# Performance work log

Hardware: AMD Instinct MI355X
Metric: run time of the kernel (lower is better)

## Reference

```python
import jax, jax.numpy as jnp
import numpy as np

N_I = 500_000   # 'indivi' nodes (dst)
N_H = 200_000   # 'house' nodes
F_I = 32        # indivi feature dim
F_H = 16        # house feature dim
EF = 8          # edge_attr dim
E1 = 2_000_000  # house->indivi edges
E2 = 2_000_000  # indivi->indivi edges


def setup_inputs() -> dict:
    key = jax.random.key(0)
    ks = jax.random.split(key, 16)
    return {
        "x_indivi": jax.random.normal(ks[0], (N_I, F_I), jnp.float32),
        "x_house": jax.random.normal(ks[1], (N_H, F_H), jnp.float32),
        "edge_attr_h2i": jax.random.normal(ks[2], (E1, EF), jnp.float32),
        "edge_attr_i2i": jax.random.normal(ks[3], (E2, EF), jnp.float32),
        "W_edge_h2i": jax.random.normal(ks[4], (F_H, EF), jnp.float32) * 0.1,
        "b_edge_h2i": jax.random.normal(ks[5], (F_H,), jnp.float32) * 0.1,
        "W_edge_i2i": jax.random.normal(ks[6], (F_I, EF), jnp.float32) * 0.1,
        "b_edge_i2i": jax.random.normal(ks[7], (F_I,), jnp.float32) * 0.1,
        "W_root_h2i": jax.random.normal(ks[8], (1, F_I), jnp.float32) * 0.1,
        "bias_h2i": jax.random.normal(ks[9], (1,), jnp.float32) * 0.1,
        "W_root_i2i": jax.random.normal(ks[10], (1, F_I), jnp.float32) * 0.1,
        "bias_i2i": jax.random.normal(ks[11], (1,), jnp.float32) * 0.1,
        "src_h2i": jax.random.randint(ks[12], (E1,), 0, N_H, jnp.int32),
        "dst_h2i": jax.random.randint(ks[13], (E1,), 0, N_I, jnp.int32),
        "src_i2i": jax.random.randint(ks[14], (E2,), 0, N_I, jnp.int32),
        "dst_i2i": jax.random.randint(ks[15], (E2,), 0, N_I, jnp.int32),
    }


def _nnconv(x_src, x_dst, edge_attr, src, dst, W_edge, b_edge, W_root, bias, num_dst):
    # Edge MLP -> per-edge weight matrix of shape [F_src, out=1], flattened to [E, F_src]
    w = edge_attr @ W_edge.T + b_edge                     # [E, F_src]
    # message_e = x_src[src_e] @ w_e  (out_channels = 1)
    msg = jnp.sum(x_src[src] * w, axis=-1, keepdims=True)  # [E, 1]
    agg = jax.ops.segment_sum(msg, dst, num_segments=num_dst)  # [N_dst, 1]
    # root transform on destination features + bias
    return agg + x_dst @ W_root.T + bias                  # [N_dst, 1]


def reference(x_indivi, x_house, edge_attr_h2i, edge_attr_i2i,
              W_edge_h2i, b_edge_h2i, W_edge_i2i, b_edge_i2i,
              W_root_h2i, bias_h2i, W_root_i2i, bias_i2i,
              src_h2i, dst_h2i, src_i2i, dst_i2i):
    out_h = _nnconv(x_house, x_indivi, edge_attr_h2i, src_h2i, dst_h2i,
                    W_edge_h2i, b_edge_h2i, W_root_h2i, bias_h2i, N_I)
    out_i = _nnconv(x_indivi, x_indivi, edge_attr_i2i, src_i2i, dst_i2i,
                    W_edge_i2i, b_edge_i2i, W_root_i2i, bias_i2i, N_I)
    # HeteroConv(aggr='sum') over the two relations targeting 'indivi'
    return out_h + out_i
```

## Files before the change

### kernel.cpp

```cpp
#include <hip/hip_runtime.h>

#define N_I 500000
#define N_H 200000
#define E1  2000000
#define E2  2000000
#define TOTAL_E (E1 + E2)

#define NB 512
#define CHUNK 2048
#define NWG ((TOTAL_E + CHUNK - 1) / CHUNK)
#define NB_RED ((N_I + 1023) / 1024)
#define WPT 8

template<int F, bool ROOT>
__global__ __launch_bounds__(256) void precompute_g(
    const float* __restrict__ x, const float* __restrict__ W, const float* __restrict__ b,
    float* __restrict__ g, int n,
    const float* __restrict__ rW1, const float* __restrict__ rW2,
    const float* __restrict__ rb1, const float* __restrict__ rb2,
    float* __restrict__ out)
{
    __shared__ float Wf[F * 8];
    __shared__ float bv[F];
    __shared__ float wr[F];

    for (int i = threadIdx.x; i < F * 8; i += 256) Wf[i] = W[i];
    if (threadIdx.x < F) {
        bv[threadIdx.x] = b[threadIdx.x];
        if (ROOT) wr[threadIdx.x] = rW1[threadIdx.x] + rW2[threadIdx.x];
    }
    __syncthreads();

    int nid = blockIdx.x * 256 + threadIdx.x;
    if (nid >= n) return;

    float xv[F];
    const float4* xp = (const float4*)(x + (size_t)nid * F);
    #pragma unroll
    for (int q = 0; q < F / 4; q++) {
        float4 v = xp[q];
        xv[q*4+0] = v.x; xv[q*4+1] = v.y; xv[q*4+2] = v.z; xv[q*4+3] = v.w;
    }

    float acc[9];
    #pragma unroll
    for (int k = 0; k < 9; k++) acc[k] = 0.f;

    #pragma unroll
    for (int j = 0; j < F; j++) {
        float4 w0 = *(const float4*)(Wf + j * 8);
        float4 w1 = *(const float4*)(Wf + j * 8 + 4);
        float xj = xv[j];
        acc[0] = fmaf(xj, w0.x, acc[0]);
        acc[1] = fmaf(xj, w0.y, acc[1]);
        acc[2] = fmaf(xj, w0.z, acc[2]);
        acc[3] = fmaf(xj, w0.w, acc[3]);
        acc[4] = fmaf(xj, w1.x, acc[4]);
        acc[5] = fmaf(xj, w1.y, acc[5]);
        acc[6] = fmaf(xj, w1.z, acc[6]);
        acc[7] = fmaf(xj, w1.w, acc[7]);
        acc[8] = fmaf(xj, bv[j], acc[8]);
    }

    float4* gp = (float4*)(g + (size_t)nid * 12);
    gp[0] = make_float4(acc[0], acc[1], acc[2], acc[3]);
    gp[1] = make_float4(acc[4], acc[5], acc[6], acc[7]);
    gp[2] = make_float4(acc[8], 0.f, 0.f, 0.f);

    if (ROOT) {
        float r = rb1[0] + rb2[0];
        #pragma unroll
        for (int j = 0; j < F; j++) r = fmaf(xv[j], wr[j], r);
        out[nid] = r;
    }
}

__device__ __forceinline__ void edge_msg(
    int t,
    const int* __restrict__ src1, const int* __restrict__ dst1,
    const float* __restrict__ ea1, const float* __restrict__ g1,
    const int* __restrict__ src2, const int* __restrict__ dst2,
    const float* __restrict__ ea2, const float* __restrict__ g2,
    int& d_out, float& m_out)
{
    const int* srcp; const int* dstp; const float* eap; const float* gp;
    int e;
    if (t < E1) { e = t;      srcp = src1; dstp = dst1; eap = ea1; gp = g1; }
    else        { e = t - E1; srcp = src2; dstp = dst2; eap = ea2; gp = g2; }

    int s = srcp[e];
    d_out = dstp[e];
    const float4* ap = (const float4*)(eap + (size_t)e * 8);
    float4 a0 = ap[0];
    float4 a1 = ap[1];
    const float4* gr = (const float4*)(gp + (size_t)s * 12);
    float4 ga = gr[0];
    float4 gb = gr[1];
    float4 gc = gr[2];

    float msg = gc.x;
    msg = fmaf(a0.x, ga.x, msg);
    msg = fmaf(a0.y, ga.y, msg);
    msg = fmaf(a0.z, ga.z, msg);
    msg = fmaf(a0.w, ga.w, msg);
    msg = fmaf(a1.x, gb.x, msg);
    msg = fmaf(a1.y, gb.y, msg);
    msg = fmaf(a1.z, gb.z, msg);
    msg = fmaf(a1.w, gb.w, msg);
    m_out = msg;
}

__global__ __launch_bounds__(256) void hist_kernel(
    const int* __restrict__ dst1, const int* __restrict__ dst2,
    int* __restrict__ H)
{
    __shared__ int hist[NB];
    for (int i = threadIdx.x; i < NB; i += 256) hist[i] = 0;
    __syncthreads();

    int base = blockIdx.x * CHUNK;
    #pragma unroll
    for (int it = 0; it < CHUNK / 256; ++it) {
        int t = base + it * 256 + threadIdx.x;
        if (t < TOTAL_E) {
            int d = (t < E1) ? dst1[t] : dst2[t - E1];
            atomicAdd(&hist[d >> 10], 1);
        }
    }
    __syncthreads();
    for (int i = threadIdx.x; i < NB; i += 256) H[blockIdx.x * NB + i] = hist[i];
}

__global__ __launch_bounds__(256) void scan_cols_kernel(int* __restrict__ H,
                                                        int* __restrict__ total)
{
    __shared__ int sums[256];
    int b = blockIdx.x;
    int tid = threadIdx.x;

    int vals[WPT];
    int s = 0;
    #pragma unroll
    for (int k = 0; k < WPT; k++) {
        int w = tid * WPT + k;
        vals[k] = (w < NWG) ? H[w * NB + b] : 0;
        s += vals[k];
    }
    sums[tid] = s;
    __syncthreads();
    for (int off = 1; off < 256; off <<= 1) {
        int t = (tid >= off) ? sums[tid - off] : 0;
        __syncthreads();
        sums[tid] += t;
        __syncthreads();
    }
    int run = sums[tid] - s;
    #pragma unroll
    for (int k = 0; k < WPT; k++) {
        int w = tid * WPT + k;
        if (w < NWG) H[w * NB + b] = run;
        run += vals[k];
    }
    if (tid == 255) total[b] = sums[255];
}

__global__ __launch_bounds__(512) void scan_base_kernel(const int* __restrict__ total,
                                                        int* __restrict__ base)
{
    __shared__ int v[512];
    int tid = threadIdx.x;
    int orig = total[tid];
    v[tid] = orig;
    __syncthreads();
    for (int off = 1; off < 512; off <<= 1) {
        int t = (tid >= off) ? v[tid - off] : 0;
        __syncthreads();
        v[tid] += t;
        __syncthreads();
    }
    base[tid] = v[tid] - orig;
}

__global__ __launch_bounds__(256) void scatter_msg_kernel(
    const int* __restrict__ src1, const int* __restrict__ dst1,
    const float* __restrict__ ea1, const float* __restrict__ g1,
    const int* __restrict__ src2, const int* __restrict__ dst2,
    const float* __restrict__ ea2, const float* __restrict__ g2,
    const int* __restrict__ H, const int* __restrict__ base,
    uint2* __restrict__ pairs)
{
    __shared__ int cur[NB];
    for (int i = threadIdx.x; i < NB; i += 256)
        cur[i] = H[blockIdx.x * NB + i] + base[i];
    __syncthreads();

    int cbase = blockIdx.x * CHUNK;
    #pragma unroll
    for (int it = 0; it < CHUNK / 256; ++it) {
        int t = cbase + it * 256 + threadIdx.x;
        if (t < TOTAL_E) {
            int d; float m;
            edge_msg(t, src1, dst1, ea1, g1, src2, dst2, ea2, g2, d, m);
            int pos = atomicAdd(&cur[d >> 10], 1);
            pairs[pos] = make_uint2((unsigned)d, __float_as_uint(m));
        }
    }
}

__global__ __launch_bounds__(1024) void reduce_kernel(
    const uint2* __restrict__ pairs, const int* __restrict__ base,
    const int* __restrict__ total, float* __restrict__ out)
{
    __shared__ float acc[1024];
    if (threadIdx.x < 1024) acc[threadIdx.x] = 0.f;
    __syncthreads();

    int b = blockIdx.x;
    int start = base[b];
    int cnt = total[b];
    for (int i = threadIdx.x; i < cnt; i += 1024) {
        uint2 p = pairs[start + i];
        atomicAdd(&acc[p.x & 1023], __uint_as_float(p.y));
    }
    __syncthreads();

    int n = (b << 10) + threadIdx.x;
    if (n < N_I) out[n] += acc[threadIdx.x];
}

__global__ __launch_bounds__(256) void edge_kernel_atomic(
    const int* __restrict__ src1, const int* __restrict__ dst1,
    const float* __restrict__ ea1, const float* __restrict__ g1,
    const int* __restrict__ src2, const int* __restrict__ dst2,
    const float* __restrict__ ea2, const float* __restrict__ g2,
    float* __restrict__ out)
{
    int t = blockIdx.x * 256 + threadIdx.x;
    if (t >= TOTAL_E) return;
    int d; float m;
    edge_msg(t, src1, dst1, ea1, g1, src2, dst2, ea2, g2, d, m);
    atomicAdd(out + d, m);
}

extern "C" void kernel_launch(void* const* d_in, const int* in_sizes, int n_in,
                              void* d_out, int out_size, void* d_ws, size_t ws_size,
                              hipStream_t stream) {
    const float* x_i  = (const float*)d_in[0];
    const float* x_h  = (const float*)d_in[1];
    const float* ea_h = (const float*)d_in[2];
    const float* ea_i = (const float*)d_in[3];
    const float* We_h = (const float*)d_in[4];
    const float* be_h = (const float*)d_in[5];
    const float* We_i = (const float*)d_in[6];
    const float* be_i = (const float*)d_in[7];
    const float* Wr_h = (const float*)d_in[8];
    const float* br_h = (const float*)d_in[9];
    const float* Wr_i = (const float*)d_in[10];
    const float* br_i = (const float*)d_in[11];
    const int* src_h = (const int*)d_in[12];
    const int* dst_h = (const int*)d_in[13];
    const int* src_i = (const int*)d_in[14];
    const int* dst_i = (const int*)d_in[15];

    float* out = (float*)d_out;

    char* ws = (char*)d_ws;
    float* g_i   = (float*)ws;
    float* g_h   = (float*)(ws + 24000000);
    uint2* pairs = (uint2*)(ws + 33600000);
    int*   H     = (int*)  (ws + 65600000);
    int*   tot   = (int*)  (ws + 69601792);
    int*   bas   = (int*)  (ws + 69603840);
    const size_t WS_NEEDED = 69605888;

    precompute_g<16, false><<<(N_H + 255) / 256, 256, 0, stream>>>(
        x_h, We_h, be_h, g_h, N_H, nullptr, nullptr, nullptr, nullptr, nullptr);
    precompute_g<32, true><<<(N_I + 255) / 256, 256, 0, stream>>>(
        x_i, We_i, be_i, g_i, N_I, Wr_h, Wr_i, br_h, br_i, out);

    if (ws_size >= WS_NEEDED) {
        hist_kernel<<<NWG, 256, 0, stream>>>(dst_h, dst_i, H);
        scan_cols_kernel<<<NB, 256, 0, stream>>>(H, tot);
        scan_base_kernel<<<1, 512, 0, stream>>>(tot, bas);
        scatter_msg_kernel<<<NWG, 256, 0, stream>>>(
            src_h, dst_h, ea_h, g_h, src_i, dst_i, ea_i, g_i, H, bas, pairs);
        reduce_kernel<<<NB_RED, 1024, 0, stream>>>(pairs, bas, tot, out);
    } else {
        edge_kernel_atomic<<<(TOTAL_E + 255) / 256, 256, 0, stream>>>(
            src_h, dst_h, ea_h, g_h, src_i, dst_i, ea_i, g_i, out);
    }
}
```

Baseline: 443.3 us.

## Stage messages, locally sort scatter in LDS, split reduce with merge pass

The per-edge message is now computed in the histogram pass and written to a buffer. The scatter pass re-reads only dst and that message, counting-sorts each chunk in LDS, and then writes pairs out so that consecutive lanes hit contiguous addresses instead of scattering randomly. Buckets grow to 4096 nodes (128 buckets), and each bucket's reduction is split across 4 blocks that write partial sums, followed by a merge kernel. This targets the uncoalesced pair writes and low reduce parallelism. The cost is an extra 16MB message write and read, larger LDS use per block, and one more launch; workspace regions are reused, which relies on the order the kernels run in.

New measurement: 369.5 us. -16.7%, faster.

```diff
diff --git a/kernel.cpp b/kernel.cpp
--- a/kernel.cpp
+++ b/kernel.cpp
@@ -6,10 +6,11 @@
 #define E2  2000000
 #define TOTAL_E (E1 + E2)
 
-#define NB 512
+#define BSHIFT 12
+#define NB 128
+#define NBK ((N_I + 4095) / 4096)
 #define CHUNK 2048
 #define NWG ((TOTAL_E + CHUNK - 1) / CHUNK)
-#define NB_RED ((N_I + 1023) / 1024)
 #define WPT 8
 
 template<int F, bool ROOT>
@@ -110,12 +111,15 @@
     m_out = msg;
 }
 
-__global__ __launch_bounds__(256) void hist_kernel(
-    const int* __restrict__ dst1, const int* __restrict__ dst2,
-    int* __restrict__ H)
+__global__ __launch_bounds__(256) void msg_hist_kernel(
+    const int* __restrict__ src1, const int* __restrict__ dst1,
+    const float* __restrict__ ea1, const float* __restrict__ g1,
+    const int* __restrict__ src2, const int* __restrict__ dst2,
+    const float* __restrict__ ea2, const float* __restrict__ g2,
+    float* __restrict__ msg_out, int* __restrict__ H)
 {
     __shared__ int hist[NB];
-    for (int i = threadIdx.x; i < NB; i += 256) hist[i] = 0;
+    if (threadIdx.x < NB) hist[threadIdx.x] = 0;
     __syncthreads();
 
     int base = blockIdx.x * CHUNK;
@@ -123,12 +127,14 @@
     for (int it = 0; it < CHUNK / 256; ++it) {
         int t = base + it * 256 + threadIdx.x;
         if (t < TOTAL_E) {
-            int d = (t < E1) ? dst1[t] : dst2[t - E1];
-            atomicAdd(&hist[d >> 10], 1);
+            int d; float m;
+            edge_msg(t, src1, dst1, ea1, g1, src2, dst2, ea2, g2, d, m);
+            msg_out[t] = m;
+            atomicAdd(&hist[d >> BSHIFT], 1);
         }
     }
     __syncthreads();
-    for (int i = threadIdx.x; i < NB; i += 256) H[blockIdx.x * NB + i] = hist[i];
+    if (threadIdx.x < NB) H[blockIdx.x * NB + threadIdx.x] = hist[threadIdx.x];
 }
 
 __global__ __launch_bounds__(256) void scan_cols_kernel(int* __restrict__ H,
@@ -164,15 +170,15 @@
     if (tid == 255) total[b] = sums[255];
 }
 
-__global__ __launch_bounds__(512) void scan_base_kernel(const int* __restrict__ total,
+__global__ __launch_bounds__(128) void scan_base_kernel(const int* __restrict__ total,
                                                         int* __restrict__ base)
 {
-    __shared__ int v[512];
+    __shared__ int v[NB];
     int tid = threadIdx.x;
     int orig = total[tid];
     v[tid] = orig;
     __syncthreads();
-    for (int off = 1; off < 512; off <<= 1) {
+    for (int off = 1; off < NB; off <<= 1) {
         int t = (tid >= off) ? v[tid - off] : 0;
         __syncthreads();
         v[tid] += t;
@@ -181,51 +187,109 @@
     base[tid] = v[tid] - orig;
 }
 
-__global__ __launch_bounds__(256) void scatter_msg_kernel(
-    const int* __restrict__ src1, const int* __restrict__ dst1,
-    const float* __restrict__ ea1, const float* __restrict__ g1,
-    const int* __restrict__ src2, const int* __restrict__ dst2,
-    const float* __restrict__ ea2, const float* __restrict__ g2,
-    const int* __restrict__ H, const int* __restrict__ base,
-    uint2* __restrict__ pairs)
-{
-    __shared__ int cur[NB];
-    for (int i = threadIdx.x; i < NB; i += 256)
-        cur[i] = H[blockIdx.x * NB + i] + base[i];
+__global__ __launch_bounds__(256) void scatter_kernel(
+    const int* __restrict__ dst1, const int* __restrict__ dst2,
+    const float* __restrict__ msg, const int* __restrict__ H,
+    const int* __restrict__ base, uint2* __restrict__ pairs)
+{
+    __shared__ int cnt[NB];
+    __shared__ int sv[NB];
+    __shared__ int gbase[NB];
+    __shared__ unsigned short bkt[CHUNK];
+    __shared__ uint2 lp[CHUNK];
+
+    int tid = threadIdx.x;
+    if (tid < NB) cnt[tid] = 0;
     __syncthreads();
 
     int cbase = blockIdx.x * CHUNK;
+    int dloc[CHUNK / 256];
     #pragma unroll
     for (int it = 0; it < CHUNK / 256; ++it) {
-        int t = cbase + it * 256 + threadIdx.x;
+        int t = cbase + it * 256 + tid;
+        int d = -1;
         if (t < TOTAL_E) {
-            int d; float m;
-            edge_msg(t, src1, dst1, ea1, g1, src2, dst2, ea2, g2, d, m);
-            int pos = atomicAdd(&cur[d >> 10], 1);
-            pairs[pos] = make_uint2((unsigned)d, __float_as_uint(m));
+            d = (t < E1) ? dst1[t] : dst2[t - E1];
+            atomicAdd(&cnt[d >> BSHIFT], 1);
         }
-    }
-}
-
-__global__ __launch_bounds__(1024) void reduce_kernel(
+        dloc[it] = d;
+    }
+    __syncthreads();
+
+    int myc = 0;
+    if (tid < NB) { myc = cnt[tid]; sv[tid] = myc; }
+    __syncthreads();
+    for (int off = 1; off < NB; off <<= 1) {
+        int t = (tid < NB && tid >= off) ? sv[tid - off] : 0;
+        __syncthreads();
+        if (tid < NB) sv[tid] += t;
+        __syncthreads();
+    }
+    if (tid < NB) {
+        int loff = sv[tid] - myc;
+        gbase[tid] = H[blockIdx.x * NB + tid] + base[tid] - loff;
+        cnt[tid] = loff;
+    }
+    __syncthreads();
+
+    #pragma unroll
+    for (int it = 0; it < CHUNK / 256; ++it) {
+        int t = cbase + it * 256 + tid;
+        if (t < TOTAL_E) {
+            int d = dloc[it];
+            float m = msg[t];
+            int b = d >> BSHIFT;
+            int slot = atomicAdd(&cnt[b], 1);
+            lp[slot] = make_uint2((unsigned)d, __float_as_uint(m));
+            bkt[slot] = (unsigned short)b;
+        }
+    }
+    __syncthreads();
+
+    int nvalid = TOTAL_E - cbase;
+    if (nvalid > CHUNK) nvalid = CHUNK;
+    for (int i = tid; i < nvalid; i += 256) {
+        int b = bkt[i];
+        pairs[gbase[b] + i] = lp[i];
+    }
+}
+
+__global__ __launch_bounds__(512) void reduce_kernel(
     const uint2* __restrict__ pairs, const int* __restrict__ base,
-    const int* __restrict__ total, float* __restrict__ out)
-{
-    __shared__ float acc[1024];
-    if (threadIdx.x < 1024) acc[threadIdx.x] = 0.f;
-    __syncthreads();
-
-    int b = blockIdx.x;
+    const int* __restrict__ total, float* __restrict__ part)
+{
+    __shared__ float acc[4096];
+    for (int i = threadIdx.x; i < 4096; i += 512) acc[i] = 0.f;
+    __syncthreads();
+
+    int b = blockIdx.x >> 2;
+    int k = blockIdx.x & 3;
     int start = base[b];
     int cnt = total[b];
-    for (int i = threadIdx.x; i < cnt; i += 1024) {
+    int q = (cnt + 3) >> 2;
+    int s0 = k * q;
+    int s1 = s0 + q; if (s1 > cnt) s1 = cnt;
+
+    for (int i = s0 + threadIdx.x; i < s1; i += 512) {
         uint2 p = pairs[start + i];
-        atomicAdd(&acc[p.x & 1023], __uint_as_float(p.y));
-    }
-    __syncthreads();
-
-    int n = (b << 10) + threadIdx.x;
-    if (n < N_I) out[n] += acc[threadIdx.x];
+        atomicAdd(&acc[p.x & 4095], __uint_as_float(p.y));
+    }
+    __syncthreads();
+
+    float* dp = part + (size_t)blockIdx.x * 4096;
+    for (int i = threadIdx.x; i < 4096; i += 512) dp[i] = acc[i];
+}
+
+__global__ __launch_bounds__(256) void merge_kernel(
+    const float* __restrict__ part, float* __restrict__ out)
+{
+    int n = blockIdx.x * 256 + threadIdx.x;
+    if (n < N_I) {
+        int b = n >> BSHIFT;
+        int i = n & 4095;
+        const float* p = part + (size_t)b * 4 * 4096 + i;
+        out[n] += (p[0] + p[4096]) + (p[8192] + p[12288]);
+    }
 }
 
 __global__ __launch_bounds__(256) void edge_kernel_atomic(
@@ -267,11 +331,13 @@
     char* ws = (char*)d_ws;
     float* g_i   = (float*)ws;
     float* g_h   = (float*)(ws + 24000000);
-    uint2* pairs = (uint2*)(ws + 33600000);
-    int*   H     = (int*)  (ws + 65600000);
-    int*   tot   = (int*)  (ws + 69601792);
-    int*   bas   = (int*)  (ws + 69603840);
-    const size_t WS_NEEDED = 69605888;
+    uint2* pairs = (uint2*)ws;
+    float* msg   = (float*)(ws + 33600000);
+    float* part  = (float*)(ws + 33600000);
+    int*   H     = (int*)  (ws + 49600000);
+    int*   tot   = (int*)  (ws + 50600448);
+    int*   bas   = (int*)  (ws + 50602496);
+    const size_t WS_NEEDED = 50603008;
 
     precompute_g<16, false><<<(N_H + 255) / 256, 256, 0, stream>>>(
         x_h, We_h, be_h, g_h, N_H, nullptr, nullptr, nullptr, nullptr, nullptr);
@@ -279,12 +345,14 @@
         x_i, We_i, be_i, g_i, N_I, Wr_h, Wr_i, br_h, br_i, out);
 
     if (ws_size >= WS_NEEDED) {
-        hist_kernel<<<NWG, 256, 0, stream>>>(dst_h, dst_i, H);
+        msg_hist_kernel<<<NWG, 256, 0, stream>>>(
+            src_h, dst_h, ea_h, g_h, src_i, dst_i, ea_i, g_i, msg, H);
         scan_cols_kernel<<<NB, 256, 0, stream>>>(H, tot);
-        scan_base_kernel<<<1, 512, 0, stream>>>(tot, bas);
-        scatter_msg_kernel<<<NWG, 256, 0, stream>>>(
-            src_h, dst_h, ea_h, g_h, src_i, dst_i, ea_i, g_i, H, bas, pairs);
-        reduce_kernel<<<NB_RED, 1024, 0, stream>>>(pairs, bas, tot, out);
+        scan_base_kernel<<<1, NB, 0, stream>>>(tot, bas);
+        scatter_kernel<<<NWG, 256, 0, stream>>>(
+            dst_h, dst_i, msg, H, bas, pairs);
+        reduce_kernel<<<NBK * 4, 512, 0, stream>>>(pairs, bas, tot, part);
+        merge_kernel<<<(N_I + 255) / 256, 256, 0, stream>>>(part, out);
     } else {
         edge_kernel_atomic<<<(TOTAL_E + 255) / 256, 256, 0, stream>>>(
             src_h, dst_h, ea_h, g_h, src_i, dst_i, ea_i, g_i, out);
```
